# Optimization experiments

Measured on AMD Instinct MI355X. Metric: run time of the kernel, lower is better.

The kernel has to match this reference:

```python
import jax, jax.numpy as jnp
import numpy as np

NUM_HEADS = 8  # matches init_kwargs

def setup_inputs() -> dict:
    key = jax.random.key(0)
    ks = jax.random.split(key, 5)
    b, n, c = 8, 4096, 512
    scale_in = 1.0 / np.sqrt(c)
    return {
        'x': jax.random.normal(ks[0], (b, n, c), jnp.float32),
        'wqkv_w': jax.random.normal(ks[1], (3 * c, c), jnp.float32) * scale_in,
        'wqkv_b': jax.random.normal(ks[2], (3 * c,), jnp.float32) * 0.02,
        'wp_w': jax.random.normal(ks[3], (c, c), jnp.float32) * scale_in,
        'wp_b': jax.random.normal(ks[4], (c,), jnp.float32) * 0.02,
    }

def reference(x, wqkv_w, wqkv_b, wp_w, wp_b):
    b, n, c = x.shape
    h = NUM_HEADS
    d = c // h
    # QKV projection (torch Linear: x @ W^T + b)
    qkv = x @ wqkv_w.T + wqkv_b                      # (b, n, 3c)
    qkv = jnp.transpose(qkv.reshape(b, n, 3, c), (2, 0, 1, 3))
    q, k, v = qkv[0], qkv[1], qkv[2]                 # each (b, n, c)
    # Faithful to original: reshape (b,n,h,d) -> (b,h,n,d) is a FLAT
    # reinterpretation (torch .reshape), not a transpose.
    q = q.reshape(b, n, h, d).reshape(b, h, n, d)
    k = k.reshape(b, n, h, d).reshape(b, h, n, d)
    v = v.reshape(b, n, h, d).reshape(b, h, n, d)
    # Channel (cross-covariance) attention: contract over tokens n.
    scores = jnp.einsum('bhnd,bhne->bhde', q, k) / jnp.sqrt(jnp.float32(d))
    weights = jax.nn.softmax(scores, axis=-1)        # softmax over head_dim
    y = jnp.einsum('bhde,bhme->bhdm', weights, v)    # (b, h, d, n)
    y = jnp.transpose(y, (0, 3, 1, 2)).reshape(b, n, c)
    return y @ wp_w.T + wp_b
```

## Files before the change

### kernel.cpp

```cpp
#include <hip/hip_runtime.h>

typedef short s16x8 __attribute__((ext_vector_type(8)));
typedef float f32x4 __attribute__((ext_vector_type(4)));
typedef unsigned short us;

__device__ inline us f2bf(float f){
    union{float f;unsigned u;} v{f};
    unsigned r = v.u + 0x7fff + ((v.u>>16)&1);
    return (us)(r>>16);
}

__device__ __forceinline__ void glds16(const us* g, us* l){
    __builtin_amdgcn_global_load_lds(
        (const __attribute__((address_space(1))) unsigned int*)(g),
        (__attribute__((address_space(3))) unsigned int*)(l), 16, 0, 0);
}

__global__ void cast_all(const float* __restrict__ x, const float* __restrict__ wqkv_w,
                         const float* __restrict__ wp_w, us* __restrict__ xbf,
                         us* __restrict__ wqkvbf, us* __restrict__ wpbf){
    int i = blockIdx.x*blockDim.x + threadIdx.x;
    const float* s; us* d; int j;
    if(i < 4194304){ s = x; d = xbf; j = i; }
    else if(i < 4390912){ s = wqkv_w; d = wqkvbf; j = i - 4194304; }
    else { s = wp_w; d = wpbf; j = i - 4390912; }
    float4 f = ((const float4*)s)[j];
    ushort4 o;
    o.x = f2bf(f.x); o.y = f2bf(f.y); o.z = f2bf(f.z); o.w = f2bf(f.w);
    ((ushort4*)d)[j] = o;
}

__launch_bounds__(256,4)
__global__ void gemm_qkv(const us* __restrict__ A, const us* __restrict__ B,
                         const float* __restrict__ bias, us* __restrict__ C){
    __shared__ __attribute__((aligned(16))) us sA[128*64];
    __shared__ __attribute__((aligned(16))) us sB[128*64];
    int t = threadIdx.x;
    int id = blockIdx.x;
    int xcd = id & 7, s = id >> 3;
    int nt = s % 12, mt = xcd*32 + s/12;
    int lane = t&63, wave = t>>6, quad = lane>>4, l15 = lane&15;
    int wm = wave>>1, wn = wave&1;

    int l8 = lane>>3;
    int sw = ((lane&7) ^ l8)*8;
    const us* Ag = A + (size_t)(mt*128 + wave*32 + l8)*512 + sw;
    const us* Bg = B + (size_t)(nt*128 + wave*32 + l8)*512 + sw;
    us* sAw = &sA[(wave*32)*64];
    us* sBw = &sB[(wave*32)*64];

    f32x4 acc[4][4];
    #pragma unroll
    for(int i=0;i<4;i++)
        #pragma unroll
        for(int j=0;j<4;j++) acc[i][j] = (f32x4){0.f,0.f,0.f,0.f};

    for(int k0=0; k0<512; k0+=64){
        glds16(Ag + k0,           sAw);
        glds16(Ag + 8*512 + k0,   sAw + 8*64);
        glds16(Ag + 16*512 + k0,  sAw + 16*64);
        glds16(Ag + 24*512 + k0,  sAw + 24*64);
        glds16(Bg + k0,           sBw);
        glds16(Bg + 8*512 + k0,   sBw + 8*64);
        glds16(Bg + 16*512 + k0,  sBw + 16*64);
        glds16(Bg + 24*512 + k0,  sBw + 24*64);
        __syncthreads();
        #pragma unroll
        for(int ks=0; ks<2; ks++){
            int kc = ks*4 + quad;
            s16x8 af[4], bfr[4];
            #pragma unroll
            for(int i=0;i<4;i++){
                int r = wm*64 + i*16 + l15;
                af[i] = *(const s16x8*)&sA[r*64 + ((kc ^ (r&7))<<3)];
            }
            #pragma unroll
            for(int j=0;j<4;j++){
                int r = wn*64 + j*16 + l15;
                bfr[j] = *(const s16x8*)&sB[r*64 + ((kc ^ (r&7))<<3)];
            }
            #pragma unroll
            for(int i=0;i<4;i++)
                #pragma unroll
                for(int j=0;j<4;j++)
                    acc[i][j] = __builtin_amdgcn_mfma_f32_16x16x32_bf16(af[i], bfr[j], acc[i][j], 0,0,0);
        }
        __syncthreads();
    }

    int row0 = mt*128 + wm*64, col0 = nt*128 + wn*64;
    #pragma unroll
    for(int j=0;j<4;j++){
        int col = col0 + j*16 + l15;
        float bv = bias[col];
        #pragma unroll
        for(int i=0;i<4;i++){
            int rbase = row0 + i*16 + quad*4;
            #pragma unroll
            for(int r=0;r<4;r++)
                C[(size_t)(rbase+r)*1536 + col] = f2bf(acc[i][j][r] + bv);
        }
    }
}

__launch_bounds__(256,4)
__global__ void attn_scores_mfma(const us* __restrict__ qkv, float* __restrict__ Sp){
    __shared__ __attribute__((aligned(16))) us sQt[64*72];
    __shared__ __attribute__((aligned(16))) us sKt[64*72];
    int t = threadIdx.x;
    int kb = blockIdx.x, head = blockIdx.y;
    int lane = t & 63, w = t >> 6;
    int quad = lane >> 4, l15 = lane & 15;
    int p = t & 31;
    int d0 = (t >> 5) * 8;

    f32x4 acc[4];
    #pragma unroll
    for(int j=0;j<4;j++) acc[j] = (f32x4){0.f,0.f,0.f,0.f};

    for(int chunk=0; chunk<8; chunk++){
        int r0 = head*512 + kb*64 + chunk*8;
        const us* g = qkv + (size_t)(r0 + (p>>2))*1536 + (2*(p&3))*64 + d0;
        union{uint4 v; us h[8];} q0, q1, k0, k1;
        q0.v = *(const uint4*)g;         q1.v = *(const uint4*)(g + 64);
        k0.v = *(const uint4*)(g + 512); k1.v = *(const uint4*)(g + 576);
        #pragma unroll
        for(int j=0;j<8;j++){
            *(unsigned*)&sQt[(d0+j)*72 + 2*p] = (unsigned)q0.h[j] | ((unsigned)q1.h[j]<<16);
            *(unsigned*)&sKt[(d0+j)*72 + 2*p] = (unsigned)k0.h[j] | ((unsigned)k1.h[j]<<16);
        }
        __syncthreads();
        int d = w*16 + l15;
        #pragma unroll
        for(int ks=0; ks<2; ks++){
            int tb = ks*4 + quad;
            s16x8 af = *(const s16x8*)&sQt[d*72 + tb*8];
            #pragma unroll
            for(int jt=0; jt<4; jt++){
                int e = jt*16 + l15;
                s16x8 bfv = *(const s16x8*)&sKt[e*72 + tb*8];
                acc[jt] = __builtin_amdgcn_mfma_f32_16x16x32_bf16(af, bfv, acc[jt], 0,0,0);
            }
        }
        __syncthreads();
    }

    float* S = Sp + (size_t)(kb*64 + head)*4096;
    #pragma unroll
    for(int jt=0; jt<4; jt++){
        int e = jt*16 + l15;
        #pragma unroll
        for(int r=0; r<4; r++){
            int d = w*16 + quad*4 + r;
            S[d*64 + e] = acc[jt][r];
        }
    }
}

__global__ void softmax64(const float* __restrict__ Sp, us* __restrict__ W){
    int head = blockIdx.x>>2, part = blockIdx.x&3;
    int t = threadIdx.x;
    int d = part*16 + (t>>4), e0 = (t&15)*4;
    float4 v = {0.f,0.f,0.f,0.f};
    for(int kb=0; kb<8; kb++){
        float4 f = *(const float4*)&Sp[(size_t)(kb*64 + head)*4096 + d*64 + e0];
        v.x+=f.x; v.y+=f.y; v.z+=f.z; v.w+=f.w;
    }
    v.x*=0.125f; v.y*=0.125f; v.z*=0.125f; v.w*=0.125f;
    float m = fmaxf(fmaxf(v.x,v.y), fmaxf(v.z,v.w));
    m = fmaxf(m, __shfl_xor(m, 1));
    m = fmaxf(m, __shfl_xor(m, 2));
    m = fmaxf(m, __shfl_xor(m, 4));
    m = fmaxf(m, __shfl_xor(m, 8));
    v.x=__expf(v.x-m); v.y=__expf(v.y-m); v.z=__expf(v.z-m); v.w=__expf(v.w-m);
    float s = v.x+v.y+v.z+v.w;
    s += __shfl_xor(s, 1);
    s += __shfl_xor(s, 2);
    s += __shfl_xor(s, 4);
    s += __shfl_xor(s, 8);
    float inv = 1.f/s;
    union{uint2 u; us h[4];} o;
    o.h[0]=f2bf(v.x*inv); o.h[1]=f2bf(v.y*inv); o.h[2]=f2bf(v.z*inv); o.h[3]=f2bf(v.w*inv);
    *(uint2*)&W[(size_t)head*4096 + d*64 + e0] = o.u;
}

__launch_bounds__(256,2)
__global__ void fold(const us* __restrict__ Wsm, const us* __restrict__ wpbf,
                     us* __restrict__ Mcat){
    __shared__ us sWt[64*72];
    int t = threadIdx.x;
    int head = blockIdx.x>>2, part = blockIdx.x&3;
    int b = head>>3, h = head&7;
    int lane = t&63, w = t>>6, quad = lane>>4, l15 = lane&15;
    #pragma unroll
    for(int it=0; it<2; it++){
        int idx = it*2048 + t*8;
        int d = idx>>6, e0 = idx&63;
        union{uint4 v; us s[8];} q;
        q.v = *(const uint4*)&Wsm[(size_t)head*4096 + idx];
        #pragma unroll
        for(int j=0;j<8;j++) sWt[(e0+j)*72 + d] = q.s[j];
    }
    __syncthreads();
    #pragma unroll
    for(int i=0;i<2;i++){
        int nO = part*128 + w*32 + i*16 + l15;
        s16x8 af0 = *(const s16x8*)&wpbf[(size_t)nO*512 + h*64 + quad*8];
        s16x8 af1 = *(const s16x8*)&wpbf[(size_t)nO*512 + h*64 + 32 + quad*8];
        #pragma unroll
        for(int j=0;j<4;j++){
            s16x8 bf0 = *(const s16x8*)&sWt[(j*16+l15)*72 + quad*8];
            s16x8 bf1 = *(const s16x8*)&sWt[(j*16+l15)*72 + 32 + quad*8];
            f32x4 acc = (f32x4){0.f,0.f,0.f,0.f};
            acc = __builtin_amdgcn_mfma_f32_16x16x32_bf16(af0, bf0, acc, 0,0,0);
            acc = __builtin_amdgcn_mfma_f32_16x16x32_bf16(af1, bf1, acc, 0,0,0);
            #pragma unroll
            for(int r=0;r<4;r++){
                int row = part*128 + w*32 + i*16 + quad*4 + r;
                Mcat[((size_t)(b*512 + row))*512 + h*64 + j*16 + l15] = f2bf(acc[r]);
            }
        }
    }
}

__launch_bounds__(256,4)
__global__ void gemm_vout(const us* __restrict__ qkv, const us* __restrict__ Mcat,
                          const float* __restrict__ bias, float* __restrict__ out){
    __shared__ __attribute__((aligned(16))) us sA[128*64];
    __shared__ __attribute__((aligned(16))) us sB[128*64];
    int t = threadIdx.x;
    int id = blockIdx.x;
    int xcd = id & 7, s = id >> 3;
    int nt = s & 3, mt = xcd*32 + (s>>2);
    int b = mt>>5, mr = mt&31;
    int lane = t&63, wave = t>>6, quad = lane>>4, l15 = lane&15;
    int wm = wave>>1, wn = wave&1;

    int l8 = lane>>3;
    int sw = ((lane&7) ^ l8)*8;
    const us* Abase = qkv + ((size_t)(8*b)*512 + mr*16 + wave*4)*1536 + 1024 + l8*64 + sw;
    const us* Bbase = Mcat + ((size_t)(b*512 + nt*128 + wave*32 + l8))*512 + sw;
    us* sAw = &sA[(wave*32)*64];
    us* sBw = &sB[(wave*32)*64];

    f32x4 acc[4][4];
    #pragma unroll
    for(int i=0;i<4;i++)
        #pragma unroll
        for(int j=0;j<4;j++) acc[i][j] = (f32x4){0.f,0.f,0.f,0.f};

    for(int h=0; h<8; h++){
        const us* Ah = Abase + (size_t)h*512*1536;
        const us* Bh = Bbase + h*64;
        glds16(Ah,           sAw);
        glds16(Ah + 1536,    sAw + 8*64);
        glds16(Ah + 2*1536,  sAw + 16*64);
        glds16(Ah + 3*1536,  sAw + 24*64);
        glds16(Bh,           sBw);
        glds16(Bh + 8*512,   sBw + 8*64);
        glds16(Bh + 16*512,  sBw + 16*64);
        glds16(Bh + 24*512,  sBw + 24*64);
        __syncthreads();
        #pragma unroll
        for(int ks=0; ks<2; ks++){
            int kc = ks*4 + quad;
            s16x8 af[4], bfr[4];
            #pragma unroll
            for(int i=0;i<4;i++){
                int r = wm*64 + i*16 + l15;
                af[i] = *(const s16x8*)&sA[r*64 + ((kc ^ (r&7))<<3)];
            }
            #pragma unroll
            for(int j=0;j<4;j++){
                int r = wn*64 + j*16 + l15;
                bfr[j] = *(const s16x8*)&sB[r*64 + ((kc ^ (r&7))<<3)];
            }
            #pragma unroll
            for(int i=0;i<4;i++)
                #pragma unroll
                for(int j=0;j<4;j++)
                    acc[i][j] = __builtin_amdgcn_mfma_f32_16x16x32_bf16(af[i], bfr[j], acc[i][j], 0,0,0);
        }
        __syncthreads();
    }

    int row0 = b*4096 + mr*128 + wm*64;
    int col0 = nt*128 + wn*64;
    #pragma unroll
    for(int j=0;j<4;j++){
        int col = col0 + j*16 + l15;
        float bv = bias[col];
        #pragma unroll
        for(int i=0;i<4;i++){
            int rbase = row0 + i*16 + quad*4;
            #pragma unroll
            for(int r2=0;r2<4;r2++)
                out[(size_t)(rbase+r2)*512 + col] = acc[i][j][r2] + bv;
        }
    }
}

extern "C" void kernel_launch(void* const* d_in, const int* in_sizes, int n_in,
                              void* d_out, int out_size, void* d_ws, size_t ws_size,
                              hipStream_t stream){
    const float* x      = (const float*)d_in[0];
    const float* wqkv_w = (const float*)d_in[1];
    const float* wqkv_b = (const float*)d_in[2];
    const float* wp_w   = (const float*)d_in[3];
    const float* wp_b   = (const float*)d_in[4];

    char* ws = (char*)d_ws;
    us*    qkvbf  = (us*)(ws);
    us*    xbf    = (us*)(ws + 100663296);
    float* Spart  = (float*)(ws + 134217728);
    us*    Wsm    = (us*)(ws + 142606336);
    us*    Mcat   = (us*)(ws + 143130624);
    us*    wqkvbf = (us*)(ws + 147324928);
    us*    wpbf   = (us*)(ws + 148897792);

    cast_all<<<17408,256,0,stream>>>(x, wqkv_w, wp_w, xbf, wqkvbf, wpbf);

    gemm_qkv<<<3072,256,0,stream>>>(xbf, wqkvbf, wqkv_b, qkvbf);

    attn_scores_mfma<<<dim3(8,64),256,0,stream>>>(qkvbf, Spart);
    softmax64<<<256,256,0,stream>>>(Spart, Wsm);
    fold<<<256,256,0,stream>>>(Wsm, wpbf, Mcat);

    gemm_vout<<<1024,256,0,stream>>>(qkvbf, Mcat, wp_b, (float*)d_out);
}
```

Measured before the change: 233.3 us.

## Vectorize GEMM epilogues via swapped MFMA operands, fuse softmax into fold, prefetch scores

Both GEMMs swap the MFMA A/B operands so each lane holds four consecutive output columns, which turns the scalar strided epilogue stores into 4-wide vector stores with vector bias loads. The softmax kernel is merged into the fold kernel, removing one launch and the bf16 round trip of the softmax weights through global memory. The attention-scores kernel now register-prefetches the next chunk of Q/K while computing the current one, at the cost of extra registers. In the fused kernel each of the four part-blocks per head recomputes the same softmax, which adds redundant reads of the partial scores.

```diff
diff --git a/kernel.cpp b/kernel.cpp
--- a/kernel.cpp
+++ b/kernel.cpp
@@ -83,22 +83,26 @@
             for(int i=0;i<4;i++)
                 #pragma unroll
                 for(int j=0;j<4;j++)
-                    acc[i][j] = __builtin_amdgcn_mfma_f32_16x16x32_bf16(af[i], bfr[j], acc[i][j], 0,0,0);
+                    acc[i][j] = __builtin_amdgcn_mfma_f32_16x16x32_bf16(bfr[j], af[i], acc[i][j], 0,0,0);
         }
         __syncthreads();
     }
 
     int row0 = mt*128 + wm*64, col0 = nt*128 + wn*64;
-    #pragma unroll
-    for(int j=0;j<4;j++){
-        int col = col0 + j*16 + l15;
-        float bv = bias[col];
-        #pragma unroll
-        for(int i=0;i<4;i++){
-            int rbase = row0 + i*16 + quad*4;
-            #pragma unroll
-            for(int r=0;r<4;r++)
-                C[(size_t)(rbase+r)*1536 + col] = f2bf(acc[i][j][r] + bv);
+    float4 bv[4];
+    #pragma unroll
+    for(int j=0;j<4;j++) bv[j] = *(const float4*)&bias[col0 + j*16 + quad*4];
+    #pragma unroll
+    for(int i=0;i<4;i++){
+        size_t rb = (size_t)(row0 + i*16 + l15)*1536 + col0;
+        #pragma unroll
+        for(int j=0;j<4;j++){
+            ushort4 o;
+            o.x = f2bf(acc[i][j][0] + bv[j].x);
+            o.y = f2bf(acc[i][j][1] + bv[j].y);
+            o.z = f2bf(acc[i][j][2] + bv[j].z);
+            o.w = f2bf(acc[i][j][3] + bv[j].w);
+            *(ushort4*)&C[rb + j*16 + quad*4] = o;
         }
     }
 }
@@ -118,12 +122,19 @@
     #pragma unroll
     for(int j=0;j<4;j++) acc[j] = (f32x4){0.f,0.f,0.f,0.f};
 
-    for(int chunk=0; chunk<8; chunk++){
-        int r0 = head*512 + kb*64 + chunk*8;
-        const us* g = qkv + (size_t)(r0 + (p>>2))*1536 + (2*(p&3))*64 + d0;
-        union{uint4 v; us h[8];} q0, q1, k0, k1;
-        q0.v = *(const uint4*)g;         q1.v = *(const uint4*)(g + 64);
-        k0.v = *(const uint4*)(g + 512); k1.v = *(const uint4*)(g + 576);
+    const us* gbase = qkv + (size_t)(head*512 + kb*64 + (p>>2))*1536 + (2*(p&3))*64 + d0;
+    union U{uint4 v; us h[8];};
+    U q0,q1,k0,k1, nq0,nq1,nk0,nk1;
+    q0.v = *(const uint4*)gbase;         q1.v = *(const uint4*)(gbase + 64);
+    k0.v = *(const uint4*)(gbase + 512); k1.v = *(const uint4*)(gbase + 576);
+
+    #pragma unroll
+    for(int c=0; c<8; c++){
+        if(c<7){
+            const us* g = gbase + (size_t)(c+1)*8*1536;
+            nq0.v = *(const uint4*)g;         nq1.v = *(const uint4*)(g + 64);
+            nk0.v = *(const uint4*)(g + 512); nk1.v = *(const uint4*)(g + 576);
+        }
         #pragma unroll
         for(int j=0;j<8;j++){
             *(unsigned*)&sQt[(d0+j)*72 + 2*p] = (unsigned)q0.h[j] | ((unsigned)q1.h[j]<<16);
@@ -137,12 +148,12 @@
             s16x8 af = *(const s16x8*)&sQt[d*72 + tb*8];
             #pragma unroll
             for(int jt=0; jt<4; jt++){
-                int e = jt*16 + l15;
-                s16x8 bfv = *(const s16x8*)&sKt[e*72 + tb*8];
+                s16x8 bfv = *(const s16x8*)&sKt[(jt*16+l15)*72 + tb*8];
                 acc[jt] = __builtin_amdgcn_mfma_f32_16x16x32_bf16(af, bfv, acc[jt], 0,0,0);
             }
         }
         __syncthreads();
+        q0 = nq0; q1 = nq1; k0 = nk0; k1 = nk1;
     }
 
     float* S = Sp + (size_t)(kb*64 + head)*4096;
@@ -157,51 +168,42 @@
     }
 }
 
-__global__ void softmax64(const float* __restrict__ Sp, us* __restrict__ W){
-    int head = blockIdx.x>>2, part = blockIdx.x&3;
-    int t = threadIdx.x;
-    int d = part*16 + (t>>4), e0 = (t&15)*4;
-    float4 v = {0.f,0.f,0.f,0.f};
-    for(int kb=0; kb<8; kb++){
-        float4 f = *(const float4*)&Sp[(size_t)(kb*64 + head)*4096 + d*64 + e0];
-        v.x+=f.x; v.y+=f.y; v.z+=f.z; v.w+=f.w;
-    }
-    v.x*=0.125f; v.y*=0.125f; v.z*=0.125f; v.w*=0.125f;
-    float m = fmaxf(fmaxf(v.x,v.y), fmaxf(v.z,v.w));
-    m = fmaxf(m, __shfl_xor(m, 1));
-    m = fmaxf(m, __shfl_xor(m, 2));
-    m = fmaxf(m, __shfl_xor(m, 4));
-    m = fmaxf(m, __shfl_xor(m, 8));
-    v.x=__expf(v.x-m); v.y=__expf(v.y-m); v.z=__expf(v.z-m); v.w=__expf(v.w-m);
-    float s = v.x+v.y+v.z+v.w;
-    s += __shfl_xor(s, 1);
-    s += __shfl_xor(s, 2);
-    s += __shfl_xor(s, 4);
-    s += __shfl_xor(s, 8);
-    float inv = 1.f/s;
-    union{uint2 u; us h[4];} o;
-    o.h[0]=f2bf(v.x*inv); o.h[1]=f2bf(v.y*inv); o.h[2]=f2bf(v.z*inv); o.h[3]=f2bf(v.w*inv);
-    *(uint2*)&W[(size_t)head*4096 + d*64 + e0] = o.u;
-}
-
 __launch_bounds__(256,2)
-__global__ void fold(const us* __restrict__ Wsm, const us* __restrict__ wpbf,
-                     us* __restrict__ Mcat){
+__global__ void softfold(const float* __restrict__ Sp, const us* __restrict__ wpbf,
+                         us* __restrict__ Mcat){
     __shared__ us sWt[64*72];
     int t = threadIdx.x;
     int head = blockIdx.x>>2, part = blockIdx.x&3;
     int b = head>>3, h = head&7;
     int lane = t&63, w = t>>6, quad = lane>>4, l15 = lane&15;
-    #pragma unroll
-    for(int it=0; it<2; it++){
-        int idx = it*2048 + t*8;
-        int d = idx>>6, e0 = idx&63;
-        union{uint4 v; us s[8];} q;
-        q.v = *(const uint4*)&Wsm[(size_t)head*4096 + idx];
-        #pragma unroll
-        for(int j=0;j<8;j++) sWt[(e0+j)*72 + d] = q.s[j];
-    }
+
+    int d = t>>2, e0 = (t&3)*16;
+    float vv[16];
+    #pragma unroll
+    for(int j=0;j<16;j++) vv[j] = 0.f;
+    for(int kb=0; kb<8; kb++){
+        const float4* pp = (const float4*)&Sp[(size_t)(kb*64 + head)*4096 + d*64 + e0];
+        #pragma unroll
+        for(int q=0;q<4;q++){
+            float4 g = pp[q];
+            vv[4*q+0]+=g.x; vv[4*q+1]+=g.y; vv[4*q+2]+=g.z; vv[4*q+3]+=g.w;
+        }
+    }
+    float m = -1e30f;
+    #pragma unroll
+    for(int j=0;j<16;j++){ vv[j] *= 0.125f; m = fmaxf(m, vv[j]); }
+    m = fmaxf(m, __shfl_xor(m, 1));
+    m = fmaxf(m, __shfl_xor(m, 2));
+    float ssum = 0.f;
+    #pragma unroll
+    for(int j=0;j<16;j++){ vv[j] = __expf(vv[j]-m); ssum += vv[j]; }
+    ssum += __shfl_xor(ssum, 1);
+    ssum += __shfl_xor(ssum, 2);
+    float inv = 1.f/ssum;
+    #pragma unroll
+    for(int j=0;j<16;j++) sWt[(e0+j)*72 + d] = f2bf(vv[j]*inv);
     __syncthreads();
+
     #pragma unroll
     for(int i=0;i<2;i++){
         int nO = part*128 + w*32 + i*16 + l15;
@@ -279,23 +281,27 @@
             for(int i=0;i<4;i++)
                 #pragma unroll
                 for(int j=0;j<4;j++)
-                    acc[i][j] = __builtin_amdgcn_mfma_f32_16x16x32_bf16(af[i], bfr[j], acc[i][j], 0,0,0);
+                    acc[i][j] = __builtin_amdgcn_mfma_f32_16x16x32_bf16(bfr[j], af[i], acc[i][j], 0,0,0);
         }
         __syncthreads();
     }
 
     int row0 = b*4096 + mr*128 + wm*64;
     int col0 = nt*128 + wn*64;
-    #pragma unroll
-    for(int j=0;j<4;j++){
-        int col = col0 + j*16 + l15;
-        float bv = bias[col];
-        #pragma unroll
-        for(int i=0;i<4;i++){
-            int rbase = row0 + i*16 + quad*4;
-            #pragma unroll
-            for(int r2=0;r2<4;r2++)
-                out[(size_t)(rbase+r2)*512 + col] = acc[i][j][r2] + bv;
+    float4 bv[4];
+    #pragma unroll
+    for(int j=0;j<4;j++) bv[j] = *(const float4*)&bias[col0 + j*16 + quad*4];
+    #pragma unroll
+    for(int i=0;i<4;i++){
+        size_t rb = (size_t)(row0 + i*16 + l15)*512 + col0;
+        #pragma unroll
+        for(int j=0;j<4;j++){
+            float4 o;
+            o.x = acc[i][j][0] + bv[j].x;
+            o.y = acc[i][j][1] + bv[j].y;
+            o.z = acc[i][j][2] + bv[j].z;
+            o.w = acc[i][j][3] + bv[j].w;
+            *(float4*)&out[rb + j*16 + quad*4] = o;
         }
     }
 }
@@ -313,7 +319,6 @@
     us*    qkvbf  = (us*)(ws);
     us*    xbf    = (us*)(ws + 100663296);
     float* Spart  = (float*)(ws + 134217728);
-    us*    Wsm    = (us*)(ws + 142606336);
     us*    Mcat   = (us*)(ws + 143130624);
     us*    wqkvbf = (us*)(ws + 147324928);
     us*    wpbf   = (us*)(ws + 148897792);
@@ -323,8 +328,7 @@
     gemm_qkv<<<3072,256,0,stream>>>(xbf, wqkvbf, wqkv_b, qkvbf);
 
     attn_scores_mfma<<<dim3(8,64),256,0,stream>>>(qkvbf, Spart);
-    softmax64<<<256,256,0,stream>>>(Spart, Wsm);
-    fold<<<256,256,0,stream>>>(Wsm, wpbf, Mcat);
+    softfold<<<256,256,0,stream>>>(Spart, wpbf, Mcat);
 
     gemm_vout<<<1024,256,0,stream>>>(qkvbf, Mcat, wp_b, (float*)d_out);
 }
```

Result: slower. 242.6 us (+4.0%).
